# Kernel optimization log

Measured on AMD Instinct MI355X. Metric: run time of the kernel, lower is better.

Reference implementation:

```python
import jax, jax.numpy as jnp
import numpy as np

B = 32768
MARGIN = 0.1
P = 2.0          # norm_degree
EPS_BN = 1e-3    # BatchNorm1d eps=0.001
EPS_PD = 1e-6    # F.pairwise_distance eps


def setup_inputs() -> dict:
    key = jax.random.key(0)
    ks = jax.random.split(key, 40)
    W = lambda k, o, i: jax.random.normal(k, (o, i), jnp.float32) * 0.01
    inp = {
        'img_p': jax.random.normal(ks[0], (B, 300), jnp.float32),
        'img_n': jax.random.normal(ks[1], (B, 300), jnp.float32),
        'tag':   jax.random.normal(ks[2], (B, 300), jnp.float32),
        'lat':   jax.random.uniform(ks[3], (B, 1), jnp.float32),
        'lon':   jax.random.uniform(ks[4], (B, 1), jnp.float32),
        # fc_i_1 (Linear 300->1024 + BN)
        'Wi1': W(ks[5], 1024, 300), 'bi1': jnp.zeros(1024), 'gi1': jnp.ones(1024), 'bti1': jnp.zeros(1024),
        # fc_i_2, fc_i_3
        'Wi2': W(ks[6], 1024, 1024), 'bi2': jnp.zeros(1024),
        'Wi3': W(ks[7], 300, 1024), 'bi3': jnp.zeros(300),
        # fc_loc (Linear 2->10 + BN)
        'Wloc': W(ks[8], 10, 2), 'bloc': jnp.zeros(10), 'gloc': jnp.ones(10), 'btloc': jnp.zeros(10),
        # fc_mm_1..3 (Linear + BN), fc_mm_4
        'Wm1': W(ks[9], 1024, 310), 'bm1': jnp.zeros(1024), 'gm1': jnp.ones(1024), 'btm1': jnp.zeros(1024),
        'Wm2': W(ks[10], 1024, 1024), 'bm2': jnp.zeros(1024), 'gm2': jnp.ones(1024), 'btm2': jnp.zeros(1024),
        'Wm3': W(ks[11], 1024, 1024), 'bm3': jnp.zeros(1024), 'gm3': jnp.ones(1024), 'btm3': jnp.zeros(1024),
        'Wm4': W(ks[12], 300, 1024), 'bm4': jnp.zeros(300),
    }
    return inp


def _fc_bn_relu(x, W, b, g, beta):
    # Linear -> BatchNorm1d (training mode, biased batch stats) -> ReLU
    y = x @ W.T + b
    m = jnp.mean(y, axis=0)
    v = jnp.mean((y - m) ** 2, axis=0)
    return jax.nn.relu((y - m) * jax.lax.rsqrt(v + EPS_BN) * g + beta)


def _pairwise_distance(x, y):
    # torch F.pairwise_distance with eps=1e-6
    return jnp.sum(jnp.abs(x - y + EPS_PD) ** P, axis=1) ** (1.0 / P)


def reference(img_p, img_n, tag, lat, lon,
              Wi1, bi1, gi1, bti1, Wi2, bi2, Wi3, bi3,
              Wloc, bloc, gloc, btloc,
              Wm1, bm1, gm1, btm1, Wm2, bm2, gm2, btm2,
              Wm3, bm3, gm3, btm3, Wm4, bm4):
    def img_branch(x):
        x = _fc_bn_relu(x, Wi1, bi1, gi1, bti1)
        x = x @ Wi2.T + bi2
        x = x @ Wi3.T + bi3
        return x
    p = img_branch(img_p)   # [B, 300]
    n = img_branch(img_n)   # [B, 300] (separate BN batch stats, as in torch)
    loc = jnp.concatenate([lat, lon], axis=1)           # [B, 2]
    loc = _fc_bn_relu(loc, Wloc, bloc, gloc, btloc)     # [B, 10]
    a = jnp.concatenate([loc, tag], axis=1)             # [B, 310]
    a = _fc_bn_relu(a, Wm1, bm1, gm1, btm1)
    a = _fc_bn_relu(a, Wm2, bm2, gm2, btm2)
    a = _fc_bn_relu(a, Wm3, bm3, gm3, btm3)
    a = a @ Wm4.T + bm4                                 # [B, 300]
    d_tp = _pairwise_distance(a, p)
    d_tn = _pairwise_distance(a, n)
    # vectorized replacement for the per-element python count loop
    correct = jnp.sum(d_tn - d_tp > MARGIN).astype(jnp.int32).reshape(1)
    return (p, n, a, correct)
```

## Files before the change

### kernel.cpp

```cpp
#include <hip/hip_runtime.h>

typedef _Float16 f16;
typedef _Float16 half8 __attribute__((ext_vector_type(8)));
typedef float f32x4 __attribute__((ext_vector_type(4)));

__device__ __forceinline__ void gl_lds16(const void* g, void* l) {
  __builtin_amdgcn_global_load_lds(
      (__attribute__((address_space(1))) void*)(size_t)g,
      (__attribute__((address_space(3))) void*)l, 16, 0, 0);
}

template <int EPI, int BNA>
__global__ __launch_bounds__(512, 2) void gemm256_k(
    const f16* __restrict__ A, int Ksteps, int KP,
    void* __restrict__ outp, int ldOut, int Ncols,
    float2* __restrict__ partial, int r1, int kz, int oz,
    const f16* __restrict__ B0, const float* __restrict__ bias0,
    const f16* __restrict__ sc0, const f16* __restrict__ sh0,
    const f16* __restrict__ B1, const float* __restrict__ bias1,
    const f16* __restrict__ sc1, const f16* __restrict__ sh1) {
  __shared__ char smem[135168];

  const int t = threadIdx.x;
  const int lane = t & 63;
  const int wave = t >> 6;
  const int wm = wave >> 2, wn = wave & 3;
  const int l16 = lane & 15, lg = lane >> 4;

  int bx = blockIdx.x, by = blockIdx.y;
  {
    const int nwg = gridDim.x * gridDim.y;
    const int wg = bx + gridDim.x * by;
    const int cpx = nwg >> 3;
    const int newid = (wg & 7) * cpx + (wg >> 3);
    bx = newid % gridDim.x;
    by = newid / gridDim.x;
  }
  const int m0 = by * 256;
  const int n0 = bx * 256;

  const f16* Bw = (by >= r1) ? B1 : B0;
  const float* bias = (by >= r1) ? bias1 : bias0;
  const f16* scH = (by >= r1) ? sc1 : sc0;
  const f16* shH = (by >= r1) ? sh1 : sh0;
  const f16* Az = A + (size_t)blockIdx.z * kz;
  Bw += (size_t)blockIdx.z * kz;

  f32x4 acc[8][4] = {};

  const int rA = t >> 2;
  const int g16 = ((t & 3) ^ ((t >> 3) & 3)) * 16;
  const size_t rstep = (size_t)128 * KP * 2;
  const char* gA = (const char*)Az + (size_t)(m0 + rA) * KP * 2 + g16;
  const char* gB = (const char*)Bw + (size_t)(n0 + rA) * KP * 2 + g16;

  auto stage = [&](int slot, int kt) {
    const char* pA = gA + (size_t)kt * 64;
    const char* pB = gB + (size_t)kt * 64;
    char* d = smem + slot * 32768 + t * 16;
    gl_lds16(pA, d);
    gl_lds16(pA + rstep, d + 8192);
    gl_lds16(pB, d + 16384);
    gl_lds16(pB + rstep, d + 24576);
  };

  if constexpr (BNA) {
    if (t < 128)
      gl_lds16((const char*)scH + t * 16, smem + 131072 + t * 16);
    else if (t < 256)
      gl_lds16((const char*)shH + (t - 128) * 16, smem + 133120 + (t - 128) * 16);
  }
  stage(0, 0);
  if (Ksteps > 1) stage(1, 1);
  if (Ksteps > 2) stage(2, 2);

  const int xsw = (lg ^ ((l16 >> 1) & 3)) << 4;
  const int oA0 = (wm * 128 + l16) * 64 + xsw;
  const int oB0 = (wn * 64 + l16) * 64 + xsw;

  for (int kt = 0; kt < Ksteps; ++kt) {
    if (kt + 3 < Ksteps) {
      stage((kt + 3) & 3, kt + 3);
      asm volatile("s_waitcnt vmcnt(12)" ::: "memory");
    } else if (kt + 3 == Ksteps) {
      asm volatile("s_waitcnt vmcnt(8)" ::: "memory");
    } else if (kt + 2 == Ksteps) {
      asm volatile("s_waitcnt vmcnt(4)" ::: "memory");
    } else {
      asm volatile("s_waitcnt vmcnt(0)" ::: "memory");
    }
    __builtin_amdgcn_s_barrier();
    asm volatile("" ::: "memory");

    const char* bufA = smem + (kt & 3) * 32768;
    const char* bufB = bufA + 16384;
    half8 af[8], bf[4];
#pragma unroll
    for (int m = 0; m < 8; ++m) af[m] = *(const half8*)(bufA + oA0 + m * 1024);
#pragma unroll
    for (int n = 0; n < 4; ++n) bf[n] = *(const half8*)(bufB + oB0 + n * 1024);
    if constexpr (BNA) {
      const half8 scv = *(const half8*)(smem + 131072 + kt * 64 + lg * 16);
      const half8 shv = *(const half8*)(smem + 133120 + kt * 64 + lg * 16);
      const half8 zeroh = {};
#pragma unroll
      for (int m = 0; m < 8; ++m)
        af[m] = __builtin_elementwise_max((half8)(af[m] * scv + shv), zeroh);
    }
    __builtin_amdgcn_s_setprio(1);
#pragma unroll
    for (int m = 0; m < 8; ++m)
#pragma unroll
      for (int n = 0; n < 4; ++n)
        acc[m][n] = __builtin_amdgcn_mfma_f32_16x16x32_f16(af[m], bf[n], acc[m][n], 0, 0, 0);
    __builtin_amdgcn_s_setprio(0);
    asm volatile("" ::: "memory");
    __builtin_amdgcn_s_barrier();
    asm volatile("" ::: "memory");
  }

  __syncthreads();

  float* const swv = (float*)smem + wave * 1152;
  float biasv[4];
#pragma unroll
  for (int n = 0; n < 4; ++n) {
    const int c = n0 + wn * 64 + n * 16 + l16;
    biasv[n] = (bias != nullptr && c < Ncols) ? bias[c] : 0.f;
  }
  float cs[4] = {}, cq[4] = {};
  const int rowr = lane >> 2;
  const int colc = (lane & 3) << 4;

#pragma unroll
  for (int m = 0; m < 8; ++m) {
#pragma unroll
    for (int n = 0; n < 4; ++n)
#pragma unroll
      for (int r = 0; r < 4; ++r) {
        const float v = acc[m][n][r] + biasv[n];
        swv[(lg * 4 + r) * 68 + n * 16 + l16] = v;
        if constexpr (EPI == 0) {
          cs[n] += v;
          cq[n] += v * v;
        }
      }
    asm volatile("s_waitcnt lgkmcnt(0)" ::: "memory");
    const float* sp = swv + rowr * 68 + colc;
    const int grow = m0 + wm * 128 + m * 16 + rowr;
    if constexpr (EPI == 2) {
      float* rp = (float*)outp + (size_t)blockIdx.z * oz + (size_t)grow * ldOut;
#pragma unroll
      for (int j = 0; j < 4; ++j) {
        const int c = n0 + wn * 64 + colc + j * 4;
        const f32x4 v = *(const f32x4*)(sp + j * 4);
        if (c + 3 < Ncols) {
          *(f32x4*)(rp + c) = v;
        } else {
#pragma unroll
          for (int e = 0; e < 4; ++e)
            if (c + e < Ncols) rp[c + e] = v[e];
        }
      }
    } else {
      f16* dp = (f16*)outp + (size_t)grow * ldOut + n0 + wn * 64 + colc;
      const f32x4 v0 = *(const f32x4*)(sp);
      const f32x4 v1 = *(const f32x4*)(sp + 4);
      const f32x4 v2 = *(const f32x4*)(sp + 8);
      const f32x4 v3 = *(const f32x4*)(sp + 12);
      half8 h0, h1;
#pragma unroll
      for (int e = 0; e < 4; ++e) {
        h0[e] = (f16)v0[e];
        h0[4 + e] = (f16)v1[e];
        h1[e] = (f16)v2[e];
        h1[4 + e] = (f16)v3[e];
      }
      *(half8*)dp = h0;
      *(half8*)(dp + 8) = h1;
    }
    asm volatile("s_waitcnt lgkmcnt(0)" ::: "memory");
  }

  if constexpr (EPI == 0) {
    float2* pp = partial + ((size_t)(by * 2 + wm) * 4 + lg) * 1024 + n0 + wn * 64 + l16;
#pragma unroll
    for (int n = 0; n < 4; ++n) pp[n * 16] = make_float2(cs[n], cq[n]);
  }
}

__global__ void bn_red_k(const float2* __restrict__ partial, float2* __restrict__ part2) {
  const int c = blockIdx.x * 256 + threadIdx.x;
  const int chunk = blockIdx.y;
  const float2* p = partial + (size_t)chunk * 64 * 1024 + c;
  float s = 0.f, q = 0.f;
#pragma unroll 4
  for (int i = 0; i < 64; ++i) {
    float2 v = p[(size_t)i * 1024];
    s += v.x;
    q += v.y;
  }
  part2[(size_t)chunk * 1024 + c] = make_float2(s, q);
}

__global__ void bn_fin_k(const float2* __restrict__ part2, int chunkStart, int nchunks,
                         const float* __restrict__ g, const float* __restrict__ beta,
                         f16* __restrict__ scH, f16* __restrict__ shH, float invB) {
  const int c = blockIdx.x * 256 + threadIdx.x;
  float s = 0.f, q = 0.f;
  const float2* p = part2 + (size_t)chunkStart * 1024 + c;
  for (int i = 0; i < nchunks; ++i) {
    float2 v = p[(size_t)i * 1024];
    s += v.x;
    q += v.y;
  }
  float m = s * invB;
  float var = q * invB - m * m;
  float sc = rsqrtf(var + 1e-3f) * g[c];
  scH[c] = (f16)sc;
  shH[c] = (f16)(beta[c] - m * sc);
}

__global__ void bn_fin3_k(const float2* __restrict__ part2, int cps, float invB,
                          const float* __restrict__ g0, const float* __restrict__ b0,
                          f16* __restrict__ so0, f16* __restrict__ sh0,
                          const float* __restrict__ g1, const float* __restrict__ b1,
                          f16* __restrict__ so1, f16* __restrict__ sh1,
                          const float* __restrict__ g2, const float* __restrict__ b2,
                          f16* __restrict__ so2, f16* __restrict__ sh2) {
  const int j = blockIdx.y;
  const float* g = j == 0 ? g0 : (j == 1 ? g1 : g2);
  const float* bt = j == 0 ? b0 : (j == 1 ? b1 : b2);
  f16* so = j == 0 ? so0 : (j == 1 ? so1 : so2);
  f16* sh = j == 0 ? sh0 : (j == 1 ? sh1 : sh2);
  const int c = blockIdx.x * 256 + threadIdx.x;
  float s = 0.f, q = 0.f;
  const float2* p = part2 + (size_t)j * cps * 1024 + c;
  for (int i = 0; i < cps; ++i) {
    float2 v = p[(size_t)i * 1024];
    s += v.x;
    q += v.y;
  }
  float m = s * invB;
  float var = q * invB - m * m;
  float sc = rsqrtf(var + 1e-3f) * g[c];
  so[c] = (f16)sc;
  sh[c] = (f16)(bt[c] - m * sc);
}

__global__ void cvt_all_k(const float* __restrict__ Wi1, const float* __restrict__ Wm1,
                          const float* __restrict__ Wi3, const float* __restrict__ Wm2,
                          const float* __restrict__ Wm3, const float* __restrict__ Wm4,
                          f16* __restrict__ Wi1p, f16* __restrict__ Wm1p,
                          f16* __restrict__ Wi3p, f16* __restrict__ Wm2p,
                          f16* __restrict__ Wm3p, f16* __restrict__ Wm4p) {
  const int k = blockIdx.x * 256 + threadIdx.x;
  const int row = blockIdx.y;
  const float* src;
  f16* dst;
  int n, K, KP, Nreal;
  if (row < 2048) {
    KP = 384;
    if (row < 1024) { src = Wi1; dst = Wi1p; n = row; K = 300; Nreal = 1024; }
    else { src = Wm1; dst = Wm1p; n = row - 1024; K = 310; Nreal = 1024; }
  } else {
    KP = 1024;
    if (row < 2560) { src = Wi3; dst = Wi3p; n = row - 2048; K = 1024; Nreal = 300; }
    else if (row < 3584) { src = Wm2; dst = Wm2p; n = row - 2560; K = 1024; Nreal = 1024; }
    else if (row < 4608) { src = Wm3; dst = Wm3p; n = row - 3584; K = 1024; Nreal = 1024; }
    else { src = Wm4; dst = Wm4p; n = row - 4608; K = 1024; Nreal = 300; }
  }
  if (k >= KP) return;
  float v = (n < Nreal && k < K) ? src[(size_t)n * K + k] : 0.f;
  dst[(size_t)n * KP + k] = (f16)v;
}

__global__ void cvt_wT_k(const float* __restrict__ W, f16* __restrict__ Wt) {
  __shared__ f16 tile[64][65];
  const int bx = blockIdx.x * 64, by = blockIdx.y * 64;
  const int tc = threadIdx.x & 63, tr = threadIdx.x >> 6;
#pragma unroll
  for (int r = tr; r < 64; r += 4)
    tile[r][tc] = (f16)W[(size_t)(by + r) * 1024 + bx + tc];
  __syncthreads();
#pragma unroll
  for (int r = tr; r < 64; r += 4)
    Wt[(size_t)(bx + r) * 1024 + by + tc] = tile[tc][r];
}

__global__ void cvt_in_k(const float* __restrict__ ip, const float* __restrict__ in_,
                         const float* __restrict__ tg, f16* __restrict__ Ain, int B) {
  const int gid = blockIdx.x * 256 + threadIdx.x;
  const int row = gid / 48;
  const int c0 = (gid - row * 48) * 8;
  if (row >= B) return;
  half8 vp = {}, vn = {}, vm = {};
  const float* rp = ip + (size_t)row * 300;
  const float* rn = in_ + (size_t)row * 300;
  const float* rt = tg + (size_t)row * 300;
#pragma unroll
  for (int e = 0; e < 8; ++e) {
    const int c = c0 + e;
    if (c < 300) {
      vp[e] = (f16)rp[c];
      vn[e] = (f16)rn[c];
    }
    if (c >= 10 && c < 310) vm[e] = (f16)rt[c - 10];
  }
  const size_t o = (size_t)row * 384 + c0;
  *(half8*)(Ain + o) = vp;
  *(half8*)(Ain + (size_t)B * 384 + o) = vn;
  *(half8*)(Ain + (size_t)2 * B * 384 + o) = vm;
}

__global__ void fold_red_k(const float* __restrict__ pf, f16* __restrict__ Wf) {
  const int i = blockIdx.x * 256 + threadIdx.x;
  float s = 0.f;
#pragma unroll
  for (int z = 0; z < 8; ++z) s += pf[(size_t)z * 524288 + i];
  Wf[i] = (f16)s;
}

__global__ void bfold_k(const f16* __restrict__ Wi3p, const float* __restrict__ bi2,
                        const float* __restrict__ bi3, float* __restrict__ bf) {
  const int n = blockIdx.x;
  const int t = threadIdx.x;
  float s = 0.f;
  for (int j = t; j < 1024; j += 256) s += (float)Wi3p[(size_t)n * 1024 + j] * bi2[j];
#pragma unroll
  for (int off = 32; off; off >>= 1) s += __shfl_xor(s, off);
  __shared__ float red[4];
  if ((t & 63) == 0) red[t >> 6] = s;
  __syncthreads();
  if (t == 0) bf[n] = red[0] + red[1] + red[2] + red[3] + (n < 300 ? bi3[n] : 0.f);
}

__global__ void loc_stats_k(const float* __restrict__ lat, const float* __restrict__ lon,
                            const float* __restrict__ Wloc, const float* __restrict__ bloc,
                            float* __restrict__ partial) {
  const int t = threadIdx.x;
  const int row = blockIdx.x * 256 + t;
  float la = lat[row], lo = lon[row];
  float s[10], q[10];
#pragma unroll
  for (int j = 0; j < 10; ++j) {
    float y = la * Wloc[j * 2] + lo * Wloc[j * 2 + 1] + bloc[j];
    s[j] = y;
    q[j] = y * y;
  }
#pragma unroll
  for (int j = 0; j < 10; ++j)
    for (int off = 32; off; off >>= 1) {
      s[j] += __shfl_xor(s[j], off);
      q[j] += __shfl_xor(q[j], off);
    }
  __shared__ float red[4][20];
  const int wave = t >> 6, lane = t & 63;
  if (lane == 0) {
#pragma unroll
    for (int j = 0; j < 10; ++j) {
      red[wave][j] = s[j];
      red[wave][10 + j] = q[j];
    }
  }
  __syncthreads();
  if (t < 20) partial[blockIdx.x * 20 + t] = red[0][t] + red[1][t] + red[2][t] + red[3][t];
}

__global__ void loc_fin_k(const float* __restrict__ partial, int nblk,
                          const float* __restrict__ g, const float* __restrict__ beta,
                          float2* __restrict__ ss, float invB) {
  int t = threadIdx.x;
  if (t < 10) {
    float s = 0.f, q = 0.f;
    for (int b = 0; b < nblk; ++b) {
      s += partial[b * 20 + t];
      q += partial[b * 20 + 10 + t];
    }
    float m = s * invB;
    float var = q * invB - m * m;
    float sc = rsqrtf(var + 1e-3f) * g[t];
    ss[t] = make_float2(sc, beta[t] - m * sc);
  }
}

__global__ void loc_write_k(const float* __restrict__ lat, const float* __restrict__ lon,
                            const float* __restrict__ Wloc, const float* __restrict__ bloc,
                            const float2* __restrict__ ss, f16* __restrict__ Am) {
  const int row = blockIdx.x * 256 + threadIdx.x;
  float la = lat[row], lo = lon[row];
  f16* dst = Am + (size_t)row * 384;
#pragma unroll
  for (int j = 0; j < 10; ++j) {
    float y = la * Wloc[j * 2] + lo * Wloc[j * 2 + 1] + bloc[j];
    float2 sv = ss[j];
    dst[j] = (f16)fmaxf(y * sv.x + sv.y, 0.f);
  }
}

__global__ void count_k(const float* __restrict__ P, const float* __restrict__ Nn,
                        const float* __restrict__ Aa, int B, int* __restrict__ cnt) {
  const int gw = (blockIdx.x * blockDim.x + threadIdx.x) >> 6;
  const int lane = threadIdx.x & 63;
  const int nw = (gridDim.x * blockDim.x) >> 6;
  int local = 0;
  for (int row = gw; row < B; row += nw) {
    const float* ar = Aa + (size_t)row * 300;
    const float* pr = P + (size_t)row * 300;
    const float* nr = Nn + (size_t)row * 300;
    float sp = 0.f, sn = 0.f;
    for (int e = lane; e < 300; e += 64) {
      float av = ar[e];
      float d1 = av - pr[e] + 1e-6f;
      float d2 = av - nr[e] + 1e-6f;
      sp += d1 * d1;
      sn += d2 * d2;
    }
#pragma unroll
    for (int off = 32; off; off >>= 1) {
      sp += __shfl_xor(sp, off);
      sn += __shfl_xor(sn, off);
    }
    if (lane == 0 && (sqrtf(sn) - sqrtf(sp) > 0.1f)) ++local;
  }
  if (lane == 0 && local) atomicAdd(cnt, local);
}

__global__ void zero_i32(int* p) {
  if (threadIdx.x == 0 && blockIdx.x == 0) *p = 0;
}
__global__ void write_cnt_k(const int* c, float* o) {
  if (threadIdx.x == 0 && blockIdx.x == 0) *o = (float)(*c);
}

extern "C" void kernel_launch(void* const* d_in, const int* in_sizes, int n_in,
                              void* d_out, int out_size, void* d_ws, size_t ws_size,
                              hipStream_t stream) {
  const float* img_p = (const float*)d_in[0];
  const float* img_n = (const float*)d_in[1];
  const float* tag = (const float*)d_in[2];
  const float* lat = (const float*)d_in[3];
  const float* lon = (const float*)d_in[4];
  const float* Wi1 = (const float*)d_in[5];
  const float* bi1 = (const float*)d_in[6];
  const float* gi1 = (const float*)d_in[7];
  const float* bti1 = (const float*)d_in[8];
  const float* Wi2 = (const float*)d_in[9];
  const float* bi2 = (const float*)d_in[10];
  const float* Wi3 = (const float*)d_in[11];
  const float* bi3 = (const float*)d_in[12];
  const float* Wloc = (const float*)d_in[13];
  const float* bloc = (const float*)d_in[14];
  const float* gloc = (const float*)d_in[15];
  const float* btloc = (const float*)d_in[16];
  const float* Wm1 = (const float*)d_in[17];
  const float* bm1 = (const float*)d_in[18];
  const float* gm1 = (const float*)d_in[19];
  const float* btm1 = (const float*)d_in[20];
  const float* Wm2 = (const float*)d_in[21];
  const float* bm2 = (const float*)d_in[22];
  const float* gm2 = (const float*)d_in[23];
  const float* btm2 = (const float*)d_in[24];
  const float* Wm3 = (const float*)d_in[25];
  const float* bm3 = (const float*)d_in[26];
  const float* gm3 = (const float*)d_in[27];
  const float* btm3 = (const float*)d_in[28];
  const float* Wm4 = (const float*)d_in[29];
  const float* bm4 = (const float*)d_in[30];

  const int B = in_sizes[3];
  const int MT = B / 256;
  float* out = (float*)d_out;
  float* outP = out;
  float* outN = out + (size_t)B * 300;
  float* outA = out + (size_t)2 * B * 300;
  float* outC = out + (size_t)3 * B * 300;

  char* w = (char*)d_ws;
  auto alloc = [&](size_t bytes) {
    char* p = w;
    w += (bytes + 255) & ~(size_t)255;
    return p;
  };

  f16* Wi1p = (f16*)alloc((size_t)1024 * 384 * 2);
  f16* Wm1p = (f16*)alloc((size_t)1024 * 384 * 2);
  f16* Wi2T = (f16*)alloc((size_t)1024 * 1024 * 2);
  f16* Wi3p = (f16*)alloc((size_t)512 * 1024 * 2);
  f16* Wm2p = (f16*)alloc((size_t)1024 * 1024 * 2);
  f16* Wm3p = (f16*)alloc((size_t)1024 * 1024 * 2);
  f16* Wm4p = (f16*)alloc((size_t)512 * 1024 * 2);
  f16* Wfold = (f16*)alloc((size_t)512 * 1024 * 2);
  float* bfold = (float*)alloc(512 * 4);
  f16* ssT = (f16*)alloc(10 * 1024 * 2);
  f16 *scP1 = ssT, *shP1 = ssT + 1024, *scN1 = ssT + 2048, *shN1 = ssT + 3072;
  f16 *scM1 = ssT + 4096, *shM1 = ssT + 5120, *scM2 = ssT + 6144, *shM2 = ssT + 7168;
  f16 *scM3 = ssT + 8192, *shM3 = ssT + 9216;
  float* locpart = (float*)alloc((size_t)(B / 256) * 20 * 4);
  float2* locss = (float2*)alloc(16 * 8);
  int* cnt = (int*)alloc(256);
  f16* Ain = (f16*)alloc((size_t)3 * B * 384 * 2);
  f16* Am = Ain + (size_t)2 * B * 384;
  f16* ACT0 = (f16*)alloc((size_t)3 * B * 1024 * 2);
  f16* ACT0m = ACT0 + (size_t)2 * B * 1024;
  f16* ACT1m = (f16*)alloc((size_t)B * 1024 * 2);
  float2* part = (float2*)alloc((size_t)3072 * 1024 * 8);
  float* partF = (float*)part;
  float2* part2 = (float2*)alloc((size_t)48 * 1024 * 8);
  (void)ws_size;
  (void)out_size;
  (void)n_in;

  const float invB = 1.f / (float)B;
  const int BIG = 1 << 30;

  cvt_all_k<<<dim3(4, 5120), 256, 0, stream>>>(Wi1, Wm1, Wi3, Wm2, Wm3, Wm4,
                                               Wi1p, Wm1p, Wi3p, Wm2p, Wm3p, Wm4p);
  cvt_wT_k<<<dim3(16, 16), 256, 0, stream>>>(Wi2, Wi2T);
  cvt_in_k<<<dim3(B * 48 / 256), 256, 0, stream>>>(img_p, img_n, tag, Ain, B);

  loc_stats_k<<<dim3(B / 256), 256, 0, stream>>>(lat, lon, Wloc, bloc, locpart);
  loc_fin_k<<<dim3(1), 64, 0, stream>>>(locpart, B / 256, gloc, btloc, locss, invB);
  loc_write_k<<<dim3(B / 256), 256, 0, stream>>>(lat, lon, Wloc, bloc, locss, Am);

  bfold_k<<<dim3(512), 256, 0, stream>>>(Wi3p, bi2, bi3, bfold);
  gemm256_k<2, 0><<<dim3(4, 2, 8), 512, 0, stream>>>(
      Wi3p, 4, 1024, partF, 1024, 1024, nullptr, BIG, 128, 524288,
      Wi2T, nullptr, nullptr, nullptr, Wi2T, nullptr, nullptr, nullptr);
  fold_red_k<<<dim3(2048), 256, 0, stream>>>(partF, Wfold);

  gemm256_k<0, 0><<<dim3(4, 3 * MT), 512, 0, stream>>>(
      Ain, 12, 384, ACT0, 1024, 1024, part, 2 * MT, 0, 0,
      Wi1p, bi1, nullptr, nullptr, Wm1p, bm1, nullptr, nullptr);
  bn_red_k<<<dim3(4, 48), 256, 0, stream>>>(part, part2);
  bn_fin3_k<<<dim3(4, 3), 256, 0, stream>>>(
      part2, 16, invB,
      gi1, bti1, scP1, shP1, gi1, bti1, scN1, shN1, gm1, btm1, scM1, shM1);

  gemm256_k<2, 1><<<dim3(2, 2 * MT), 512, 0, stream>>>(
      ACT0, 32, 1024, outP, 300, 300, part, MT, 0, 0,
      Wfold, bfold, scP1, shP1, Wfold, bfold, scN1, shN1);

  gemm256_k<0, 1><<<dim3(4, MT), 512, 0, stream>>>(
      ACT0m, 32, 1024, ACT1m, 1024, 1024, part, BIG, 0, 0,
      Wm2p, bm2, scM1, shM1, Wm2p, bm2, scM1, shM1);
  bn_red_k<<<dim3(4, 16), 256, 0, stream>>>(part, part2);
  bn_fin_k<<<dim3(4), 256, 0, stream>>>(part2, 0, 16, gm2, btm2, scM2, shM2, invB);
  gemm256_k<0, 1><<<dim3(4, MT), 512, 0, stream>>>(
      ACT1m, 32, 1024, ACT0, 1024, 1024, part, BIG, 0, 0,
      Wm3p, bm3, scM2, shM2, Wm3p, bm3, scM2, shM2);
  bn_red_k<<<dim3(4, 16), 256, 0, stream>>>(part, part2);
  bn_fin_k<<<dim3(4), 256, 0, stream>>>(part2, 0, 16, gm3, btm3, scM3, shM3, invB);
  gemm256_k<2, 1><<<dim3(2, MT), 512, 0, stream>>>(
      ACT0, 32, 1024, outA, 300, 300, part, BIG, 0, 0,
      Wm4p, bm4, scM3, shM3, Wm4p, bm4, scM3, shM3);

  zero_i32<<<1, 64, 0, stream>>>(cnt);
  count_k<<<dim3(1024), 256, 0, stream>>>(outP, outN, outA, B, cnt);
  write_cnt_k<<<1, 64, 0, stream>>>(cnt, outC);
}
```

Measured before the change: 740.5 us.

## Split GEMM k-step into two phases interleaving global loads with MFMA

Restructures the main GEMM loop so each k-step issues the A-tile global-to-LDS prefetch before the first half of the MFMAs and the B-tile prefetch after it. LDS reads for B are split into two halves, with barriers placed between the phases. The goal is to spread memory traffic across the compute and shorten barrier stalls. It drops the Ksteps>1/>2 guards on the prologue, so small K could read out of range, and the waitcnt bookkeeping becomes more fragile.

```diff
diff --git a/kernel.cpp b/kernel.cpp
--- a/kernel.cpp
+++ b/kernel.cpp
@@ -71,37 +71,38 @@
       gl_lds16((const char*)shH + (t - 128) * 16, smem + 133120 + (t - 128) * 16);
   }
   stage(0, 0);
-  if (Ksteps > 1) stage(1, 1);
-  if (Ksteps > 2) stage(2, 2);
+  stage(1, 1);
+  stage(2, 2);
+  asm volatile("s_waitcnt vmcnt(8)" ::: "memory");
+  __builtin_amdgcn_s_barrier();
+  asm volatile("" ::: "memory");
 
   const int xsw = (lg ^ ((l16 >> 1) & 3)) << 4;
   const int oA0 = (wm * 128 + l16) * 64 + xsw;
   const int oB0 = (wn * 64 + l16) * 64 + xsw;
 
   for (int kt = 0; kt < Ksteps; ++kt) {
-    if (kt + 3 < Ksteps) {
-      stage((kt + 3) & 3, kt + 3);
-      asm volatile("s_waitcnt vmcnt(12)" ::: "memory");
-    } else if (kt + 3 == Ksteps) {
-      asm volatile("s_waitcnt vmcnt(8)" ::: "memory");
-    } else if (kt + 2 == Ksteps) {
-      asm volatile("s_waitcnt vmcnt(4)" ::: "memory");
-    } else {
-      asm volatile("s_waitcnt vmcnt(0)" ::: "memory");
-    }
-    __builtin_amdgcn_s_barrier();
-    asm volatile("" ::: "memory");
-
     const char* bufA = smem + (kt & 3) * 32768;
     const char* bufB = bufA + 16384;
-    half8 af[8], bf[4];
+    half8 af[8], bf0, bf1, scv, shv;
 #pragma unroll
     for (int m = 0; m < 8; ++m) af[m] = *(const half8*)(bufA + oA0 + m * 1024);
-#pragma unroll
-    for (int n = 0; n < 4; ++n) bf[n] = *(const half8*)(bufB + oB0 + n * 1024);
+    bf0 = *(const half8*)(bufB + oB0);
+    bf1 = *(const half8*)(bufB + oB0 + 1024);
     if constexpr (BNA) {
-      const half8 scv = *(const half8*)(smem + 131072 + kt * 64 + lg * 16);
-      const half8 shv = *(const half8*)(smem + 133120 + kt * 64 + lg * 16);
+      scv = *(const half8*)(smem + 131072 + kt * 64 + lg * 16);
+      shv = *(const half8*)(smem + 133120 + kt * 64 + lg * 16);
+    }
+    if (kt + 3 < Ksteps) {
+      const char* pA = gA + (size_t)(kt + 3) * 64;
+      char* d = smem + ((kt + 3) & 3) * 32768 + t * 16;
+      gl_lds16(pA, d);
+      gl_lds16(pA + rstep, d + 8192);
+    }
+    asm volatile("" ::: "memory");
+    __builtin_amdgcn_s_barrier();
+    asm volatile("s_waitcnt lgkmcnt(0)" ::: "memory");
+    if constexpr (BNA) {
       const half8 zeroh = {};
 #pragma unroll
       for (int m = 0; m < 8; ++m)
@@ -109,14 +110,34 @@
     }
     __builtin_amdgcn_s_setprio(1);
 #pragma unroll
-    for (int m = 0; m < 8; ++m)
-#pragma unroll
-      for (int n = 0; n < 4; ++n)
-        acc[m][n] = __builtin_amdgcn_mfma_f32_16x16x32_f16(af[m], bf[n], acc[m][n], 0, 0, 0);
+    for (int m = 0; m < 8; ++m) {
+      acc[m][0] = __builtin_amdgcn_mfma_f32_16x16x32_f16(af[m], bf0, acc[m][0], 0, 0, 0);
+      acc[m][1] = __builtin_amdgcn_mfma_f32_16x16x32_f16(af[m], bf1, acc[m][1], 0, 0, 0);
+    }
     __builtin_amdgcn_s_setprio(0);
+    half8 bf2 = *(const half8*)(bufB + oB0 + 2048);
+    half8 bf3 = *(const half8*)(bufB + oB0 + 3072);
+    if (kt + 3 < Ksteps) {
+      const char* pB = gB + (size_t)(kt + 3) * 64;
+      char* d = smem + ((kt + 3) & 3) * 32768 + t * 16;
+      gl_lds16(pB, d + 16384);
+      gl_lds16(pB + rstep, d + 24576);
+      asm volatile("s_waitcnt vmcnt(8)" ::: "memory");
+    } else if (kt == Ksteps - 3) {
+      asm volatile("s_waitcnt vmcnt(4)" ::: "memory");
+    } else if (kt == Ksteps - 2) {
+      asm volatile("s_waitcnt vmcnt(0)" ::: "memory");
+    }
     asm volatile("" ::: "memory");
     __builtin_amdgcn_s_barrier();
-    asm volatile("" ::: "memory");
+    asm volatile("s_waitcnt lgkmcnt(0)" ::: "memory");
+    __builtin_amdgcn_s_setprio(1);
+#pragma unroll
+    for (int m = 0; m < 8; ++m) {
+      acc[m][2] = __builtin_amdgcn_mfma_f32_16x16x32_f16(af[m], bf2, acc[m][2], 0, 0, 0);
+      acc[m][3] = __builtin_amdgcn_mfma_f32_16x16x32_f16(af[m], bf3, acc[m][3], 0, 0, 0);
+    }
+    __builtin_amdgcn_s_setprio(0);
   }
 
   __syncthreads();
```

After: 712.1 us. 3.8% less time.
